# Kernel optimization log

Measured on AMD Instinct MI355X. Metric: run time of the kernel, lower is better.

The kernel has to match this reference:

```python
import jax, jax.numpy as jnp
import numpy as np

N, D = 16384, 2048

def setup_inputs() -> dict:
    key = jax.random.key(0)
    k1, k2, k3 = jax.random.split(key, 3)
    x1 = jax.random.normal(k1, (N, D), dtype=jnp.float32)
    x2 = jax.random.normal(k2, (N, D), dtype=jnp.float32)
    w = jax.random.normal(k3, (D,), dtype=jnp.float32)
    return {"x1": x1, "x2": x2, "w": w}

def reference(x1, x2, w):
    # per-row attention scores: s_k[i] = dot(x_k[i], w)
    s1 = x1 @ w  # [N]
    s2 = x2 @ w  # [N]
    # alpha_1 = exp(s1)/(exp(s1)+exp(s2)) == sigmoid(s1 - s2) (numerically stable)
    alpha1 = jax.nn.sigmoid(s1 - s2)  # [N]
    alpha2 = 1.0 - alpha1
    fused = alpha1[:, None] * x1 + alpha2[:, None] * x2  # [N, D]
    alpha = jnp.stack([alpha1, alpha2], axis=1)  # [N, 2], detached in original
    return fused, alpha
```

## Files before the change

kernel.cpp:

```cpp
#include <hip/hip_runtime.h>


#define NROWS 16384
#define DCOLS 2048

__global__ __launch_bounds__(256) void attn_fuse_kernel(
    const float* __restrict__ x1,
    const float* __restrict__ x2,
    const float* __restrict__ w,
    float* __restrict__ fused,
    float* __restrict__ alpha)
{
    const int row = blockIdx.x;
    const int t = threadIdx.x;

    const float4* x1v = (const float4*)(x1 + (size_t)row * DCOLS);
    const float4* x2v = (const float4*)(x2 + (size_t)row * DCOLS);
    const float4* wv  = (const float4*)w;

    float4 a0 = x1v[t];
    float4 a1 = x1v[t + 256];
    float4 b0 = x2v[t];
    float4 b1 = x2v[t + 256];
    float4 w0 = wv[t];
    float4 w1 = wv[t + 256];

    float p = (a0.x - b0.x) * w0.x + (a0.y - b0.y) * w0.y
            + (a0.z - b0.z) * w0.z + (a0.w - b0.w) * w0.w
            + (a1.x - b1.x) * w1.x + (a1.y - b1.y) * w1.y
            + (a1.z - b1.z) * w1.z + (a1.w - b1.w) * w1.w;

    #pragma unroll
    for (int off = 32; off > 0; off >>= 1)
        p += __shfl_down(p, off, 64);

    __shared__ float wave_sum[4];
    const int wave = t >> 6;
    const int lane = t & 63;
    if (lane == 0) wave_sum[wave] = p;
    __syncthreads();
    const float d = wave_sum[0] + wave_sum[1] + wave_sum[2] + wave_sum[3];

    const float a1g = 1.0f / (1.0f + expf(-d));

    float4 f0, f1;
    f0.x = b0.x + a1g * (a0.x - b0.x);
    f0.y = b0.y + a1g * (a0.y - b0.y);
    f0.z = b0.z + a1g * (a0.z - b0.z);
    f0.w = b0.w + a1g * (a0.w - b0.w);
    f1.x = b1.x + a1g * (a1.x - b1.x);
    f1.y = b1.y + a1g * (a1.y - b1.y);
    f1.z = b1.z + a1g * (a1.z - b1.z);
    f1.w = b1.w + a1g * (a1.w - b1.w);

    float4* outv = (float4*)(fused + (size_t)row * DCOLS);
    outv[t] = f0;
    outv[t + 256] = f1;

    if (t == 0) {
        alpha[(size_t)row * 2]     = a1g;
        alpha[(size_t)row * 2 + 1] = 1.0f - a1g;
    }
}

extern "C" void kernel_launch(void* const* d_in, const int* in_sizes, int n_in,
                              void* d_out, int out_size, void* d_ws, size_t ws_size,
                              hipStream_t stream)
{
    const float* x1 = (const float*)d_in[0];
    const float* x2 = (const float*)d_in[1];
    const float* w  = (const float*)d_in[2];

    float* fused = (float*)d_out;
    float* alpha = fused + (size_t)NROWS * DCOLS;

    attn_fuse_kernel<<<NROWS, 256, 0, stream>>>(x1, x2, w, fused, alpha);
}
```

Baseline: 304.6 us.

## Map one row per wavefront with deeper loads and nontemporal stores

Each 64-lane wavefront now handles a whole row, so the block reduction through shared memory and the barrier are replaced by an xor shuffle reduction. Each lane issues 8 vector loads per input, which raises the number of memory requests in flight, and outputs use nontemporal stores to avoid polluting the cache. The grid shrinks to a quarter of the blocks, and register pressure rises from holding 24 vectors per lane.

```diff
diff --git a/kernel.cpp b/kernel.cpp
--- a/kernel.cpp
+++ b/kernel.cpp
@@ -3,6 +3,10 @@
 
 #define NROWS 16384
 #define DCOLS 2048
+#define NBLOCKS (NROWS / 4)
+
+typedef float f32x4 __attribute__((ext_vector_type(4)));
+typedef float f32x2 __attribute__((ext_vector_type(2)));
 
 __global__ __launch_bounds__(256) void attn_fuse_kernel(
     const float* __restrict__ x1,
@@ -11,55 +15,52 @@
     float* __restrict__ fused,
     float* __restrict__ alpha)
 {
-    const int row = blockIdx.x;
-    const int t = threadIdx.x;
+    const int lane = threadIdx.x & 63;
+    const int row  = (blockIdx.x << 2) + (threadIdx.x >> 6);
 
-    const float4* x1v = (const float4*)(x1 + (size_t)row * DCOLS);
-    const float4* x2v = (const float4*)(x2 + (size_t)row * DCOLS);
-    const float4* wv  = (const float4*)w;
+    const f32x4* __restrict__ x1v = (const f32x4*)(x1 + (size_t)row * DCOLS);
+    const f32x4* __restrict__ x2v = (const f32x4*)(x2 + (size_t)row * DCOLS);
+    const f32x4* __restrict__ wv  = (const f32x4*)w;
 
-    float4 a0 = x1v[t];
-    float4 a1 = x1v[t + 256];
-    float4 b0 = x2v[t];
-    float4 b1 = x2v[t + 256];
-    float4 w0 = wv[t];
-    float4 w1 = wv[t + 256];
+    f32x4 a[8], b[8], wr[8];
+    #pragma unroll
+    for (int i = 0; i < 8; ++i) a[i] = x1v[lane + (i << 6)];
+    #pragma unroll
+    for (int i = 0; i < 8; ++i) b[i] = x2v[lane + (i << 6)];
+    #pragma unroll
+    for (int i = 0; i < 8; ++i) wr[i] = wv[lane + (i << 6)];
 
-    float p = (a0.x - b0.x) * w0.x + (a0.y - b0.y) * w0.y
-            + (a0.z - b0.z) * w0.z + (a0.w - b0.w) * w0.w
-            + (a1.x - b1.x) * w1.x + (a1.y - b1.y) * w1.y
-            + (a1.z - b1.z) * w1.z + (a1.w - b1.w) * w1.w;
+    float p = 0.0f;
+    #pragma unroll
+    for (int i = 0; i < 8; ++i) {
+        p = fmaf(a[i].x - b[i].x, wr[i].x, p);
+        p = fmaf(a[i].y - b[i].y, wr[i].y, p);
+        p = fmaf(a[i].z - b[i].z, wr[i].z, p);
+        p = fmaf(a[i].w - b[i].w, wr[i].w, p);
+    }
 
     #pragma unroll
-    for (int off = 32; off > 0; off >>= 1)
-        p += __shfl_down(p, off, 64);
+    for (int off = 1; off < 64; off <<= 1)
+        p += __shfl_xor(p, off, 64);
 
-    __shared__ float wave_sum[4];
-    const int wave = t >> 6;
-    const int lane = t & 63;
-    if (lane == 0) wave_sum[wave] = p;
-    __syncthreads();
-    const float d = wave_sum[0] + wave_sum[1] + wave_sum[2] + wave_sum[3];
+    const float a1g = 1.0f / (1.0f + expf(-p));
 
-    const float a1g = 1.0f / (1.0f + expf(-d));
+    f32x4* __restrict__ outv = (f32x4*)(fused + (size_t)row * DCOLS);
+    #pragma unroll
+    for (int i = 0; i < 8; ++i) {
+        f32x4 f;
+        f.x = fmaf(a1g, a[i].x - b[i].x, b[i].x);
+        f.y = fmaf(a1g, a[i].y - b[i].y, b[i].y);
+        f.z = fmaf(a1g, a[i].z - b[i].z, b[i].z);
+        f.w = fmaf(a1g, a[i].w - b[i].w, b[i].w);
+        __builtin_nontemporal_store(f, outv + lane + (i << 6));
+    }
 
-    float4 f0, f1;
-    f0.x = b0.x + a1g * (a0.x - b0.x);
-    f0.y = b0.y + a1g * (a0.y - b0.y);
-    f0.z = b0.z + a1g * (a0.z - b0.z);
-    f0.w = b0.w + a1g * (a0.w - b0.w);
-    f1.x = b1.x + a1g * (a1.x - b1.x);
-    f1.y = b1.y + a1g * (a1.y - b1.y);
-    f1.z = b1.z + a1g * (a1.z - b1.z);
-    f1.w = b1.w + a1g * (a1.w - b1.w);
-
-    float4* outv = (float4*)(fused + (size_t)row * DCOLS);
-    outv[t] = f0;
-    outv[t + 256] = f1;
-
-    if (t == 0) {
-        alpha[(size_t)row * 2]     = a1g;
-        alpha[(size_t)row * 2 + 1] = 1.0f - a1g;
+    if (lane == 0) {
+        f32x2 al;
+        al.x = a1g;
+        al.y = 1.0f - a1g;
+        __builtin_nontemporal_store(al, (f32x2*)(alpha + (size_t)row * 2));
     }
 }
 
@@ -74,5 +75,5 @@
     float* fused = (float*)d_out;
     float* alpha = fused + (size_t)NROWS * DCOLS;
 
-    attn_fuse_kernel<<<NROWS, 256, 0, stream>>>(x1, x2, w, fused, alpha);
+    attn_fuse_kernel<<<NBLOCKS, 256, 0, stream>>>(x1, x2, w, fused, alpha);
 }
```

Result: slower. 325.9 us (+7.0%).

## Process eight rows per block with register double-buffered prefetch of next row

Applied to the files above, without the earlier changes.

Each block now handles eight consecutive rows instead of one, loading w once per block and prefetching the next row's x1/x2 into a second register buffer while the current row is reduced and written. The block count drops from 16384 to 2048. The aim is to hide global load latency behind the reduction and barrier, and to amortize w loads and block launch overhead. In exchange it uses more registers and runs fewer blocks, which lowers the memory-level parallelism available from many concurrently resident blocks. The double-buffered shared wave_sum avoids needing a second barrier per row.

```diff
diff --git a/kernel.cpp b/kernel.cpp
--- a/kernel.cpp
+++ b/kernel.cpp
@@ -3,6 +3,10 @@
 
 #define NROWS 16384
 #define DCOLS 2048
+#define RPB 8
+#define NBLOCKS (NROWS / RPB)
+
+typedef float f32x4 __attribute__((ext_vector_type(4)));
 
 __global__ __launch_bounds__(256) void attn_fuse_kernel(
     const float* __restrict__ x1,
@@ -11,55 +15,79 @@
     float* __restrict__ fused,
     float* __restrict__ alpha)
 {
-    const int row = blockIdx.x;
     const int t = threadIdx.x;
+    const int wave = t >> 6;
+    const int lane = t & 63;
+    const size_t row0 = (size_t)blockIdx.x * RPB;
 
-    const float4* x1v = (const float4*)(x1 + (size_t)row * DCOLS);
-    const float4* x2v = (const float4*)(x2 + (size_t)row * DCOLS);
-    const float4* wv  = (const float4*)w;
+    const f32x4* __restrict__ wv = (const f32x4*)w;
+    const f32x4 w0 = wv[t];
+    const f32x4 w1 = wv[t + 256];
 
-    float4 a0 = x1v[t];
-    float4 a1 = x1v[t + 256];
-    float4 b0 = x2v[t];
-    float4 b1 = x2v[t + 256];
-    float4 w0 = wv[t];
-    float4 w1 = wv[t + 256];
+    __shared__ float wave_sum[2][4];
 
-    float p = (a0.x - b0.x) * w0.x + (a0.y - b0.y) * w0.y
-            + (a0.z - b0.z) * w0.z + (a0.w - b0.w) * w0.w
-            + (a1.x - b1.x) * w1.x + (a1.y - b1.y) * w1.y
-            + (a1.z - b1.z) * w1.z + (a1.w - b1.w) * w1.w;
+    f32x4 a0[2], a1[2], b0[2], b1[2];
+
+    {
+        const f32x4* __restrict__ x1v = (const f32x4*)(x1 + row0 * DCOLS);
+        const f32x4* __restrict__ x2v = (const f32x4*)(x2 + row0 * DCOLS);
+        a0[0] = x1v[t]; a1[0] = x1v[t + 256];
+        b0[0] = x2v[t]; b1[0] = x2v[t + 256];
+    }
 
     #pragma unroll
-    for (int off = 32; off > 0; off >>= 1)
-        p += __shfl_down(p, off, 64);
+    for (int r = 0; r < RPB; ++r) {
+        const int cur = r & 1;
+        const int nxt = cur ^ 1;
 
-    __shared__ float wave_sum[4];
-    const int wave = t >> 6;
-    const int lane = t & 63;
-    if (lane == 0) wave_sum[wave] = p;
-    __syncthreads();
-    const float d = wave_sum[0] + wave_sum[1] + wave_sum[2] + wave_sum[3];
+        if (r + 1 < RPB) {
+            const f32x4* __restrict__ x1v =
+                (const f32x4*)(x1 + (row0 + r + 1) * DCOLS);
+            const f32x4* __restrict__ x2v =
+                (const f32x4*)(x2 + (row0 + r + 1) * DCOLS);
+            a0[nxt] = x1v[t]; a1[nxt] = x1v[t + 256];
+            b0[nxt] = x2v[t]; b1[nxt] = x2v[t + 256];
+        }
 
-    const float a1g = 1.0f / (1.0f + expf(-d));
+        float p = 0.0f;
+        p = fmaf(a0[cur].x - b0[cur].x, w0.x, p);
+        p = fmaf(a0[cur].y - b0[cur].y, w0.y, p);
+        p = fmaf(a0[cur].z - b0[cur].z, w0.z, p);
+        p = fmaf(a0[cur].w - b0[cur].w, w0.w, p);
+        p = fmaf(a1[cur].x - b1[cur].x, w1.x, p);
+        p = fmaf(a1[cur].y - b1[cur].y, w1.y, p);
+        p = fmaf(a1[cur].z - b1[cur].z, w1.z, p);
+        p = fmaf(a1[cur].w - b1[cur].w, w1.w, p);
 
-    float4 f0, f1;
-    f0.x = b0.x + a1g * (a0.x - b0.x);
-    f0.y = b0.y + a1g * (a0.y - b0.y);
-    f0.z = b0.z + a1g * (a0.z - b0.z);
-    f0.w = b0.w + a1g * (a0.w - b0.w);
-    f1.x = b1.x + a1g * (a1.x - b1.x);
-    f1.y = b1.y + a1g * (a1.y - b1.y);
-    f1.z = b1.z + a1g * (a1.z - b1.z);
-    f1.w = b1.w + a1g * (a1.w - b1.w);
+        #pragma unroll
+        for (int off = 32; off > 0; off >>= 1)
+            p += __shfl_down(p, off, 64);
 
-    float4* outv = (float4*)(fused + (size_t)row * DCOLS);
-    outv[t] = f0;
-    outv[t + 256] = f1;
+        if (lane == 0) wave_sum[cur][wave] = p;
+        __syncthreads();
+        const float d = wave_sum[cur][0] + wave_sum[cur][1]
+                      + wave_sum[cur][2] + wave_sum[cur][3];
 
-    if (t == 0) {
-        alpha[(size_t)row * 2]     = a1g;
-        alpha[(size_t)row * 2 + 1] = 1.0f - a1g;
+        const float g = 1.0f / (1.0f + expf(-d));
+
+        f32x4 f0, f1;
+        f0.x = fmaf(g, a0[cur].x - b0[cur].x, b0[cur].x);
+        f0.y = fmaf(g, a0[cur].y - b0[cur].y, b0[cur].y);
+        f0.z = fmaf(g, a0[cur].z - b0[cur].z, b0[cur].z);
+        f0.w = fmaf(g, a0[cur].w - b0[cur].w, b0[cur].w);
+        f1.x = fmaf(g, a1[cur].x - b1[cur].x, b1[cur].x);
+        f1.y = fmaf(g, a1[cur].y - b1[cur].y, b1[cur].y);
+        f1.z = fmaf(g, a1[cur].z - b1[cur].z, b1[cur].z);
+        f1.w = fmaf(g, a1[cur].w - b1[cur].w, b1[cur].w);
+
+        f32x4* __restrict__ outv = (f32x4*)(fused + (row0 + r) * DCOLS);
+        outv[t] = f0;
+        outv[t + 256] = f1;
+
+        if (t == 0) {
+            alpha[(row0 + r) * 2]     = g;
+            alpha[(row0 + r) * 2 + 1] = 1.0f - g;
+        }
     }
 }
 
@@ -74,5 +102,5 @@
     float* fused = (float*)d_out;
     float* alpha = fused + (size_t)NROWS * DCOLS;
 
-    attn_fuse_kernel<<<NROWS, 256, 0, stream>>>(x1, x2, w, fused, alpha);
+    attn_fuse_kernel<<<NBLOCKS, 256, 0, stream>>>(x1, x2, w, fused, alpha);
 }
```

After: 311.3 us. 2.2% more time.
